# Performance work log

Hardware: AMD Instinct MI355X
Metric: run time of the kernel (lower is better)

The kernel has to match this reference:

```python
import jax, jax.numpy as jnp
import numpy as np

B, L, D = 4, 4096, 2048
DF = 4 * D
CAPACITY_RATIO = 0.5


def setup_inputs() -> dict:
    key = jax.random.key(0)
    ks = jax.random.split(key, 4)
    s = 0.02
    return {
        "x": jax.random.normal(ks[0], (B, L, D), dtype=jnp.float32),
        "w_r": jax.random.normal(ks[1], (D,), dtype=jnp.float32) * s,
        "b_r": jnp.zeros((), dtype=jnp.float32),
        "w1": jax.random.normal(ks[2], (D, DF), dtype=jnp.float32) * s,
        "b1": jnp.zeros((DF,), dtype=jnp.float32),
        "w2": jax.random.normal(ks[3], (DF, D), dtype=jnp.float32) * s,
        "b2": jnp.zeros((D,), dtype=jnp.float32),
    }


def reference(x, w_r, b_r, w1, b1, w2, b2):
    # MoD eval path: router scores -> top-k token indices -> gather ->
    # block (FFN) on selected tokens -> scatter back into zeros.
    b, l, d = x.shape
    k = int(l * CAPACITY_RATIO)
    scores = jnp.einsum("bld,d->bl", x, w_r) + b_r          # [B, L]
    _, idx = jax.lax.top_k(scores, k)                        # [B, k] int32
    x_sel = jnp.take_along_axis(x, idx[:, :, None], axis=1)  # [B, k, D]
    h = jax.nn.gelu(jnp.einsum("bkd,df->bkf", x_sel, w1) + b1)
    out_sel = jnp.einsum("bkf,fd->bkd", h, w2) + b2          # [B, k, D]
    batch_ix = jnp.arange(b)[:, None]                        # [B, 1]
    out = jnp.zeros_like(x).at[batch_ix, idx].set(out_sel)
    return out
```

## Files before the change

kernel.cpp:

```cpp
#include <hip/hip_runtime.h>

#define BB 4
#define LL 4096
#define DD 2048
#define DFF 8192
#define KSEL 2048
#define MROWS (BB * KSEL)

typedef __bf16 bf16x8 __attribute__((ext_vector_type(8)));
typedef float f32x4 __attribute__((ext_vector_type(4)));
typedef unsigned short u16x8 __attribute__((ext_vector_type(8)));

__device__ __forceinline__ unsigned short f2bf(float f) {
    union { float f; unsigned int u; } v; v.f = f;
    unsigned int u = v.u;
    unsigned int r = u + 0x7fffu + ((u >> 16) & 1u);
    return (unsigned short)(r >> 16);
}

__device__ __forceinline__ void gl2lds16(const void* g, void* l) {
    __builtin_amdgcn_global_load_lds(
        (const __attribute__((address_space(1))) void*)g,
        (__attribute__((address_space(3))) void*)l,
        16, 0, 0);
}

__global__ __launch_bounds__(256) void router_conv_kernel(
    const float* __restrict__ x, const float* __restrict__ wr,
    const float* __restrict__ br, float* __restrict__ scores,
    unsigned short* __restrict__ xbf)
{
    const int lane = threadIdx.x & 63;
    const int wave = threadIdx.x >> 6;
    const int tok = blockIdx.x * 4 + wave;
    const float* row = x + (long)tok * DD;
    unsigned short* orow = xbf + (long)tok * DD;
    double acc = 0.0;
#pragma unroll
    for (int it = 0; it < 4; ++it) {
        const int off = it * 512 + lane * 8;
        float4 xv = *(const float4*)(row + off);
        float4 xw = *(const float4*)(row + off + 4);
        float4 wv = *(const float4*)(wr + off);
        float4 ww = *(const float4*)(wr + off + 4);
        acc += (double)xv.x * wv.x + (double)xv.y * wv.y
             + (double)xv.z * wv.z + (double)xv.w * wv.w;
        acc += (double)xw.x * ww.x + (double)xw.y * ww.y
             + (double)xw.z * ww.z + (double)xw.w * ww.w;
        u16x8 o;
        o[0] = f2bf(xv.x); o[1] = f2bf(xv.y); o[2] = f2bf(xv.z); o[3] = f2bf(xv.w);
        o[4] = f2bf(xw.x); o[5] = f2bf(xw.y); o[6] = f2bf(xw.z); o[7] = f2bf(xw.w);
        *(u16x8*)(orow + off) = o;
    }
#pragma unroll
    for (int o = 32; o > 0; o >>= 1) acc += __shfl_down(acc, o);
    if (lane == 0) scores[tok] = (float)(acc + (double)br[0]);
}

__global__ __launch_bounds__(256) void rank_select_kernel(
    const float* __restrict__ scores, int* __restrict__ idxout,
    int* __restrict__ zidxout)
{
    __shared__ float s[LL];
    const int b = blockIdx.y;
    const float* sb = scores + b * LL;
    for (int i = threadIdx.x; i < LL; i += 256) s[i] = sb[i];
    __syncthreads();
    const int t = blockIdx.x * 256 + threadIdx.x;
    const float my = s[t];
    int rank = 0;
#pragma unroll 16
    for (int j = 0; j < LL; ++j) {
        float sj = s[j];
        rank += (sj > my) || (sj == my && j < t);
    }
    if (rank < KSEL) idxout[(b << 11) + rank] = t;
    else             zidxout[(b << 11) + rank - KSEL] = t;
}

__global__ __launch_bounds__(256) void zero_rows_kernel(
    const int* __restrict__ zidx, float* __restrict__ Out)
{
    const int m = blockIdx.x;
    const int b = m >> 11;
    const int tok = zidx[m];
    float* dst = Out + ((long)b * LL + tok) * DD;
    const int c = threadIdx.x * 8;
    float4 z = {0.f, 0.f, 0.f, 0.f};
    *(float4*)(dst + c) = z;
    *(float4*)(dst + c + 4) = z;
}

__global__ __launch_bounds__(256) void conv_transpose2_kernel(
    const float* __restrict__ W1, unsigned short* __restrict__ W1t,
    const float* __restrict__ W2, unsigned short* __restrict__ W2t)
{
    __shared__ unsigned short t[64 * 72];
    int bid = blockIdx.x;
    const float* W; unsigned short* Wt; int KR, NC, bx, by;
    if (bid < 4096) { W = W1; Wt = W1t; KR = DD; NC = DFF; bx = bid & 127; by = bid >> 7; }
    else { bid -= 4096; W = W2; Wt = W2t; KR = DFF; NC = DD; bx = bid & 31; by = bid >> 5; }
    const int n0 = bx * 64;
    const int k0 = by * 64;
    const int tid = threadIdx.x;
    const int rk = tid >> 4;
    const int cn = (tid & 15) * 4;
#pragma unroll
    for (int p = 0; p < 4; ++p) {
        const int k = rk + p * 16;
        float4 v = *(const float4*)(W + (long)(k0 + k) * NC + n0 + cn);
        t[(cn + 0) * 72 + k] = f2bf(v.x);
        t[(cn + 1) * 72 + k] = f2bf(v.y);
        t[(cn + 2) * 72 + k] = f2bf(v.z);
        t[(cn + 3) * 72 + k] = f2bf(v.w);
    }
    __syncthreads();
    const int rn = tid >> 3;
    const int ck = (tid & 7) * 8;
#pragma unroll
    for (int p = 0; p < 2; ++p) {
        const int n = rn + p * 32;
        u16x8 o = *(const u16x8*)&t[n * 72 + ck];
        *(u16x8*)(Wt + (long)(n0 + n) * KR + k0 + ck) = o;
    }
}

#define VM8 asm volatile("s_waitcnt vmcnt(8)" ::: "memory")
#define VM4 asm volatile("s_waitcnt vmcnt(4)" ::: "memory")
#define VM0 asm volatile("s_waitcnt vmcnt(0)" ::: "memory")
#define NOSTG ((void)0)
#define CFENCE asm volatile("" ::: "memory")

#define STAGE_A(BUF, q, kt) gl2lds16(ga[q] + (kt), &BUF[(q) * 4096 + wave * 512])
#define STAGE_B(BUF, q, kt) gl2lds16(gb[q] + (kt), &BUF[(q) * 4096 + wave * 512])
#define STAGE_AB(AB, BBF, kt) \
    (STAGE_A(AB, 0, kt), STAGE_A(AB, 1, kt), STAGE_B(BBF, 0, kt), STAGE_B(BBF, 1, kt))

#define TILE(ABUF, BBUF, STG, VMW) do {                                       \
    VMW;                                                                      \
    CFENCE; __builtin_amdgcn_s_barrier(); CFENCE;                             \
    const char* ab_ = (const char*)ABUF + aoff;                               \
    const char* bb_ = (const char*)BBUF + boff;                               \
    bf16x8 a0_[4], a1_[4];                                                    \
    _Pragma("unroll") for (int i_ = 0; i_ < 4; ++i_)                          \
        a0_[i_] = *(const bf16x8*)(ab_ + i_ * 1024);                          \
    _Pragma("unroll") for (int j_ = 0; j_ < 4; ++j_)                          \
        bfr[j_] = *(const bf16x8*)(bb_ + j_ * 1024);                          \
    STG;                                                                      \
    _Pragma("unroll") for (int i_ = 0; i_ < 4; ++i_)                          \
        a1_[i_] = *(const bf16x8*)(ab_ + 4096 + i_ * 1024);                   \
    __builtin_amdgcn_s_setprio(1);                                            \
    _Pragma("unroll") for (int i_ = 0; i_ < 4; ++i_)                          \
        _Pragma("unroll") for (int j_ = 0; j_ < 4; ++j_)                      \
            acc[i_][j_] = __builtin_amdgcn_mfma_f32_16x16x32_bf16(            \
                a0_[i_], bfr[j_], acc[i_][j_], 0, 0, 0);                      \
    _Pragma("unroll") for (int i_ = 0; i_ < 4; ++i_)                          \
        _Pragma("unroll") for (int j_ = 0; j_ < 4; ++j_)                      \
            acc[4 + i_][j_] = __builtin_amdgcn_mfma_f32_16x16x32_bf16(        \
                a1_[i_], bfr[j_], acc[4 + i_][j_], 0, 0, 0);                  \
    __builtin_amdgcn_s_setprio(0);                                            \
} while (0)

template <int MODE, int IND>
__global__ __launch_bounds__(512, 2) void gemm_pipe_kernel(
    const unsigned short* __restrict__ A,
    const unsigned short* __restrict__ Bt,
    const float* __restrict__ bias,
    unsigned short* __restrict__ H,
    const int* __restrict__ idx,
    float* __restrict__ Out,
    int K, int N)
{
    __shared__ unsigned short As0[8192], As1[8192], As2[8192], As3[8192];
    __shared__ unsigned short Bs0[8192], Bs1[8192], Bs2[8192], Bs3[8192];
    const int tid = threadIdx.x;
    const int lane = tid & 63;
    const int wave = tid >> 6;
    const int wm = wave >> 2;
    const int wn = wave & 3;

    const int NN = N >> 8;
    const int nwg = (int)gridDim.x;
    const int per = nwg >> 3;
    const int wg = ((int)blockIdx.x & 7) * per + ((int)blockIdx.x >> 3);
    const int gsz = 4 * NN;
    const int gidx = wg / gsz;
    const int rem = wg - gidx * gsz;
    const int pm = gidx * 4 + (rem & 3);
    const int pn = rem >> 2;
    const long m0 = (long)pm * 256;
    const long n0 = (long)pn * 256;

    const int cr = tid >> 2;
    const int cl = (tid & 3) ^ ((cr >> 1) & 3);
    const unsigned short* ga[2];
    const unsigned short* gb[2];
#pragma unroll
    for (int q = 0; q < 2; ++q) {
        const int r = q * 128 + cr;
        long ar;
        if constexpr (IND) {
            const int sel = (int)m0 + r;
            ar = (long)(sel >> 11) * LL + idx[sel];
        } else {
            ar = m0 + r;
        }
        ga[q] = A + ar * (long)K + cl * 8;
        gb[q] = Bt + (n0 + r) * (long)K + cl * 8;
    }

    const int l15 = lane & 15;
    const int lg = lane >> 4;
    const int ko = ((lg ^ ((l15 >> 1) & 3)) << 4);
    const int aoff = (wm * 128 + l15) * 64 + ko;
    const int boff = (wn * 64 + l15) * 64 + ko;

    f32x4 acc[8][4];
#pragma unroll
    for (int i = 0; i < 8; ++i)
#pragma unroll
        for (int j = 0; j < 4; ++j) {
            f32x4 z = {0.f, 0.f, 0.f, 0.f};
            acc[i][j] = z;
        }
    bf16x8 bfr[4];

    const int NT = K >> 5;

    STAGE_AB(As0, Bs0, 0);
    STAGE_AB(As1, Bs1, 32);
    STAGE_AB(As2, Bs2, 64);

    int kk = 96;
    for (int it = 0; it < (NT - 4) / 4; ++it) {
        TILE(As0, Bs0, STAGE_AB(As3, Bs3, kk), VM8); kk += 32;
        TILE(As1, Bs1, STAGE_AB(As0, Bs0, kk), VM8); kk += 32;
        TILE(As2, Bs2, STAGE_AB(As1, Bs1, kk), VM8); kk += 32;
        TILE(As3, Bs3, STAGE_AB(As2, Bs2, kk), VM8); kk += 32;
    }
    TILE(As0, Bs0, STAGE_AB(As3, Bs3, kk), VM8);
    TILE(As1, Bs1, NOSTG, VM8);
    TILE(As2, Bs2, NOSTG, VM4);
    TILE(As3, Bs3, NOSTG, VM0);

    if constexpr (MODE == 0) {
        const long rowb = m0 + wm * 128 + (lg << 2);
        const int colb = (int)n0 + wn * 64 + l15;
#pragma unroll
        for (int i = 0; i < 8; ++i) {
#pragma unroll
            for (int j = 0; j < 4; ++j) {
                const int col = colb + j * 16;
                const float bv = bias[col];
#pragma unroll
                for (int r = 0; r < 4; ++r) {
                    const long row = rowb + i * 16 + r;
                    float v = acc[i][j][r] + bv;
                    float u = v + 0.044715f * v * v * v;
                    float e = __expf(1.5957691216057308f * u);
                    float g = v - v * __builtin_amdgcn_rcpf(1.0f + e);
                    H[row * N + col] = f2bf(g);
                }
            }
        }
    } else {
        const int rowb = (int)m0 + wm * 128 + (lg << 2);
        const int colb = (int)n0 + wn * 64 + l15;
#pragma unroll
        for (int i = 0; i < 8; ++i) {
            int ob[4];
#pragma unroll
            for (int r = 0; r < 4; ++r) {
                const int row = rowb + i * 16 + r;
                const int b = row >> 11;
                const int tok = idx[(b << 11) + (row & (KSEL - 1))];
                ob[r] = (b * LL + tok) * DD;
            }
#pragma unroll
            for (int j = 0; j < 4; ++j) {
                const int col = colb + j * 16;
                const float bv = bias[col];
#pragma unroll
                for (int r = 0; r < 4; ++r)
                    Out[(long)ob[r] + col] = acc[i][j][r] + bv;
            }
        }
    }
}

extern "C" void kernel_launch(void* const* d_in, const int* in_sizes, int n_in,
                              void* d_out, int out_size, void* d_ws, size_t ws_size,
                              hipStream_t stream)
{
    const float* x  = (const float*)d_in[0];
    const float* wr = (const float*)d_in[1];
    const float* br = (const float*)d_in[2];
    const float* w1 = (const float*)d_in[3];
    const float* b1 = (const float*)d_in[4];
    const float* w2 = (const float*)d_in[5];
    const float* b2 = (const float*)d_in[6];
    float* out = (float*)d_out;

    char* ws = (char*)d_ws;
    float* scores = (float*)ws;              ws += (long)BB * LL * 4;
    int* idx  = (int*)ws;                    ws += (long)BB * KSEL * 4;
    int* zidx = (int*)ws;                    ws += (long)BB * (LL - KSEL) * 4;
    unsigned short* xbf  = (unsigned short*)ws; ws += (long)BB * LL * DD * 2;
    unsigned short* w1t  = (unsigned short*)ws; ws += (long)DFF * DD * 2;
    unsigned short* w2t  = (unsigned short*)ws; ws += (long)DD * DFF * 2;
    unsigned short* h    = (unsigned short*)ws; ws += (long)MROWS * DFF * 2;

    router_conv_kernel<<<(BB * LL) / 4, 256, 0, stream>>>(x, wr, br, scores, xbf);
    conv_transpose2_kernel<<<8192, 256, 0, stream>>>(w1, w1t, w2, w2t);
    rank_select_kernel<<<dim3(LL / 256, BB), 256, 0, stream>>>(scores, idx, zidx);
    zero_rows_kernel<<<BB * (LL - KSEL), 256, 0, stream>>>(zidx, out);
    gemm_pipe_kernel<0, 1><<<(MROWS / 256) * (DFF / 256), 512, 0, stream>>>(
        xbf, w1t, b1, h, idx, nullptr, DD, DFF);
    gemm_pipe_kernel<1, 0><<<(MROWS / 256) * (DD / 256), 512, 0, stream>>>(
        h, w2t, b2, nullptr, idx, out, DFF, DD);
}
```

Before: 964.0 us.

## Software-pipeline LDS fragment loads across K tiles to overlap with MFMA

Restructures the GEMM main loop so the next tile's A-low and B fragments are read from LDS during the current tile's MFMA phases, rather than at the start of each tile. It adds a prologue that preloads the first fragments and an epilogue tile without staging. Wait counts are tightened so the next buffer is resident before its early reads. The aim is to hide LDS read latency behind matrix math, at the cost of more live registers and a more fragile barrier and wait schedule.

```diff
diff --git a/kernel.cpp b/kernel.cpp
--- a/kernel.cpp
+++ b/kernel.cpp
@@ -136,28 +136,43 @@
 #define STAGE_AB(AB, BBF, kt) \
     (STAGE_A(AB, 0, kt), STAGE_A(AB, 1, kt), STAGE_B(BBF, 0, kt), STAGE_B(BBF, 1, kt))
 
-#define TILE(ABUF, BBUF, STG, VMW) do {                                       \
+#define TILE_F(CA, CB, NA, NB, STG, VMW) do {                                 \
     VMW;                                                                      \
     CFENCE; __builtin_amdgcn_s_barrier(); CFENCE;                             \
-    const char* ab_ = (const char*)ABUF + aoff;                               \
-    const char* bb_ = (const char*)BBUF + boff;                               \
-    bf16x8 a0_[4], a1_[4];                                                    \
-    _Pragma("unroll") for (int i_ = 0; i_ < 4; ++i_)                          \
-        a0_[i_] = *(const bf16x8*)(ab_ + i_ * 1024);                          \
-    _Pragma("unroll") for (int j_ = 0; j_ < 4; ++j_)                          \
-        bfr[j_] = *(const bf16x8*)(bb_ + j_ * 1024);                          \
+    _Pragma("unroll") for (int i_ = 0; i_ < 4; ++i_)                          \
+        a1f[i_] = *(const bf16x8*)((const char*)CA + aoff + 4096 + i_ * 1024);\
     STG;                                                                      \
-    _Pragma("unroll") for (int i_ = 0; i_ < 4; ++i_)                          \
-        a1_[i_] = *(const bf16x8*)(ab_ + 4096 + i_ * 1024);                   \
     __builtin_amdgcn_s_setprio(1);                                            \
     _Pragma("unroll") for (int i_ = 0; i_ < 4; ++i_)                          \
         _Pragma("unroll") for (int j_ = 0; j_ < 4; ++j_)                      \
             acc[i_][j_] = __builtin_amdgcn_mfma_f32_16x16x32_bf16(            \
-                a0_[i_], bfr[j_], acc[i_][j_], 0, 0, 0);                      \
+                a0f[i_], bfr[j_], acc[i_][j_], 0, 0, 0);                      \
+    __builtin_amdgcn_s_setprio(0);                                            \
+    _Pragma("unroll") for (int i_ = 0; i_ < 4; ++i_)                          \
+        a0f[i_] = *(const bf16x8*)((const char*)NA + aoff + i_ * 1024);       \
+    __builtin_amdgcn_s_setprio(1);                                            \
     _Pragma("unroll") for (int i_ = 0; i_ < 4; ++i_)                          \
         _Pragma("unroll") for (int j_ = 0; j_ < 4; ++j_)                      \
             acc[4 + i_][j_] = __builtin_amdgcn_mfma_f32_16x16x32_bf16(        \
-                a1_[i_], bfr[j_], acc[4 + i_][j_], 0, 0, 0);                  \
+                a1f[i_], bfr[j_], acc[4 + i_][j_], 0, 0, 0);                  \
+    __builtin_amdgcn_s_setprio(0);                                            \
+    _Pragma("unroll") for (int j_ = 0; j_ < 4; ++j_)                          \
+        bfr[j_] = *(const bf16x8*)((const char*)NB + boff + j_ * 1024);       \
+} while (0)
+
+#define TILE_L(CA) do {                                                       \
+    CFENCE; __builtin_amdgcn_s_barrier(); CFENCE;                             \
+    _Pragma("unroll") for (int i_ = 0; i_ < 4; ++i_)                          \
+        a1f[i_] = *(const bf16x8*)((const char*)CA + aoff + 4096 + i_ * 1024);\
+    __builtin_amdgcn_s_setprio(1);                                            \
+    _Pragma("unroll") for (int i_ = 0; i_ < 4; ++i_)                          \
+        _Pragma("unroll") for (int j_ = 0; j_ < 4; ++j_)                      \
+            acc[i_][j_] = __builtin_amdgcn_mfma_f32_16x16x32_bf16(            \
+                a0f[i_], bfr[j_], acc[i_][j_], 0, 0, 0);                      \
+    _Pragma("unroll") for (int i_ = 0; i_ < 4; ++i_)                          \
+        _Pragma("unroll") for (int j_ = 0; j_ < 4; ++j_)                      \
+            acc[4 + i_][j_] = __builtin_amdgcn_mfma_f32_16x16x32_bf16(        \
+                a1f[i_], bfr[j_], acc[4 + i_][j_], 0, 0, 0);                  \
     __builtin_amdgcn_s_setprio(0);                                            \
 } while (0)
 
@@ -223,25 +238,33 @@
             f32x4 z = {0.f, 0.f, 0.f, 0.f};
             acc[i][j] = z;
         }
-    bf16x8 bfr[4];
+    bf16x8 a0f[4], a1f[4], bfr[4];
 
     const int NT = K >> 5;
 
     STAGE_AB(As0, Bs0, 0);
     STAGE_AB(As1, Bs1, 32);
     STAGE_AB(As2, Bs2, 64);
+    VM8;
+    CFENCE; __builtin_amdgcn_s_barrier(); CFENCE;
+#pragma unroll
+    for (int i = 0; i < 4; ++i)
+        a0f[i] = *(const bf16x8*)((const char*)As0 + aoff + i * 1024);
+#pragma unroll
+    for (int j = 0; j < 4; ++j)
+        bfr[j] = *(const bf16x8*)((const char*)Bs0 + boff + j * 1024);
 
     int kk = 96;
     for (int it = 0; it < (NT - 4) / 4; ++it) {
-        TILE(As0, Bs0, STAGE_AB(As3, Bs3, kk), VM8); kk += 32;
-        TILE(As1, Bs1, STAGE_AB(As0, Bs0, kk), VM8); kk += 32;
-        TILE(As2, Bs2, STAGE_AB(As1, Bs1, kk), VM8); kk += 32;
-        TILE(As3, Bs3, STAGE_AB(As2, Bs2, kk), VM8); kk += 32;
-    }
-    TILE(As0, Bs0, STAGE_AB(As3, Bs3, kk), VM8);
-    TILE(As1, Bs1, NOSTG, VM8);
-    TILE(As2, Bs2, NOSTG, VM4);
-    TILE(As3, Bs3, NOSTG, VM0);
+        TILE_F(As0, Bs0, As1, Bs1, STAGE_AB(As3, Bs3, kk), VM4); kk += 32;
+        TILE_F(As1, Bs1, As2, Bs2, STAGE_AB(As0, Bs0, kk), VM4); kk += 32;
+        TILE_F(As2, Bs2, As3, Bs3, STAGE_AB(As1, Bs1, kk), VM4); kk += 32;
+        TILE_F(As3, Bs3, As0, Bs0, STAGE_AB(As2, Bs2, kk), VM4); kk += 32;
+    }
+    TILE_F(As0, Bs0, As1, Bs1, STAGE_AB(As3, Bs3, kk), VM4);
+    TILE_F(As1, Bs1, As2, Bs2, NOSTG, VM4);
+    TILE_F(As2, Bs2, As3, Bs3, NOSTG, VM0);
+    TILE_L(As3);
 
     if constexpr (MODE == 0) {
         const long rowb = m0 + wm * 128 + (lg << 2);
```

After: 956.6 us. No clear change (-0.8%).
